# Kernel optimization log

Hardware: AMD Instinct MI355X
Metric: run time of the kernel (lower is better)

Reference implementation:

```python
import jax, jax.numpy as jnp
import numpy as np

T, N = 8192, 1024
W_MEAN, W_VAR = 0.2, 0.4


def setup_inputs() -> dict:
    key = jax.random.key(0)
    k_x, k_w = jax.random.split(key, 2)
    x_in = jax.random.normal(k_x, (T, N), dtype=jnp.float32) * 5.0
    # w ~ U(w_mean - w_var, w_mean + w_var), matching the torch init
    w = W_MEAN - W_VAR + 2.0 * W_VAR * jax.random.uniform(k_w, (N, N), dtype=jnp.float32)
    ones = jnp.ones((N,), jnp.float32)
    return {
        "x_in": x_in,
        "w": w,
        "E_L": -54.0 * ones,
        "tau_m": 1.4 * ones,
        "G": 0.7 * ones,
        "R_I": 132.0 * ones,
        "f_v": 0.3 * ones,
        "f_I": 0.6 * ones,
        "delta_theta_s": 11.0 * ones,
        "b_s": 0.3 * ones,
        "a_v": 0.3 * ones,
        "b_v": 0.3 * ones,
        "theta_inf": -24.5 * ones,
        "delta_V": 10.0 * ones,
        "I_A": 1.6 * ones,
    }


def reference(x_in, w, E_L, tau_m, G, R_I, f_v, f_I, delta_theta_s, b_s,
              a_v, b_v, theta_inf, delta_V, I_A):
    n = w.shape[0]
    # self_recurrence_mask = ones(N,N) - eye(N)
    w_masked = w * (1.0 - jnp.eye(n, dtype=w.dtype))

    def step(carry, x):
        v, theta_s, theta_v, I_add = carry
        I = I_add @ w_masked + 0.85 * x  # [N] recurrent drive + scaled input
        v_next = v + (I * R_I - G * (v - E_L)) / tau_m
        thr = theta_s + theta_v
        spiked_soft = jax.nn.sigmoid(v_next - thr)  # surrogate spike (self.spiked)
        spiked = (v_next >= thr).astype(v.dtype)    # hard spike
        not_spiked = 1.0 - spiked
        v_reset = E_L + f_v * (v - E_L) - delta_V
        v_new = spiked * v_reset + not_spiked * v_next
        theta_s_new = (1.0 - b_s) * theta_s + spiked * delta_theta_s
        d_theta_v = a_v * (v_new - E_L) - b_v * (theta_v - theta_inf)
        theta_v_new = theta_v + not_spiked * d_theta_v
        I_add_new = (1.0 - f_I) * I_add + spiked_soft * I_A
        return (v_new, theta_s_new, theta_v_new, I_add_new), (v_new, spiked_soft)

    init = (E_L,                               # v = E_L * ones(N)
            30.0 * jnp.ones_like(E_L),         # theta_s
            jnp.ones_like(E_L),                # theta_v
            jnp.zeros_like(E_L))               # I_additive
    _, (vs, spikes) = jax.lax.scan(step, init, x_in)
    return vs, spikes  # each [T, N]
```

## Files before the change

### kernel.cpp

```cpp
#include <hip/hip_runtime.h>


#define T_STEPS 8192
#define N_NEUR  1024
#define NBLK    32
#define TPB     256
#define PSTRIDE (NBLK * N_NEUR)

typedef unsigned long long ull;

__global__ void glif_init(ull* __restrict__ buf) {
    int i = blockIdx.x * blockDim.x + threadIdx.x;
    if (i < PSTRIDE) {
        buf[i] = 0ULL;
    } else if (i < 2 * PSTRIDE) {
        buf[i] = 0xFFFFFFFF00000000ULL;
    }
}

__launch_bounds__(TPB, 1)
__global__ void glif_main(const float* __restrict__ x_in,
                          const float* __restrict__ w_p,
                          const float* __restrict__ E_L_p,
                          const float* __restrict__ tau_m_p,
                          const float* __restrict__ G_p,
                          const float* __restrict__ R_I_p,
                          const float* __restrict__ f_v_p,
                          const float* __restrict__ f_I_p,
                          const float* __restrict__ dths_p,
                          const float* __restrict__ b_s_p,
                          const float* __restrict__ a_v_p,
                          const float* __restrict__ b_v_p,
                          const float* __restrict__ th_inf_p,
                          const float* __restrict__ dV_p,
                          const float* __restrict__ I_A_p,
                          float* __restrict__ out,
                          ull* __restrict__ buf) {
    const int tid  = threadIdx.x;
    const int wv   = tid >> 6;
    const int lane = tid & 63;
    const int colL = lane & 31;
    const int col  = blockIdx.x * 32 + colL;
    const int ibase = wv * 256 + (lane >> 5) * 128;

    __shared__ float ix[N_NEUR];
    __shared__ float red[4][32];

    float wreg[128];
#pragma unroll
    for (int j = 0; j < 128; ++j) {
        int r = ibase + j;
        float wval = w_p[(size_t)r * N_NEUR + col];
        wreg[j] = (r == col) ? 0.0f : wval;
    }

    const bool own = (lane < 32);
    float E_L = 0.f, inv_tau = 0.f, Gc = 0.f, R_I = 0.f, f_v = 0.f, om_fI = 0.f;
    float dths = 0.f, om_bs = 0.f, a_v = 0.f, b_v = 0.f, th_inf = 0.f, dV = 0.f, I_A = 0.f;
    float v = 0.f, th_s = 0.f, th_v = 0.f, I_own = 0.f, xnext = 0.f;
    if (own) {
        E_L     = E_L_p[col];
        inv_tau = 1.0f / tau_m_p[col];
        Gc      = G_p[col];
        R_I     = R_I_p[col];
        f_v     = f_v_p[col];
        om_fI   = 1.0f - f_I_p[col];
        dths    = dths_p[col];
        om_bs   = 1.0f - b_s_p[col];
        a_v     = a_v_p[col];
        b_v     = b_v_p[col];
        th_inf  = th_inf_p[col];
        dV      = dV_p[col];
        I_A     = I_A_p[col];
        v = E_L; th_s = 30.0f; th_v = 1.0f; I_own = 0.0f;
        xnext = x_in[col];
    }

    float* __restrict__ vs_out = out;
    float* __restrict__ sp_out = out + (size_t)T_STEPS * N_NEUR;

    for (int t = 0; t < T_STEPS; ++t) {
        const ull* src = buf + (size_t)(t & 1) * PSTRIDE
                             + (size_t)blockIdx.x * N_NEUR + tid * 4;
        ull u0, u1, u2, u3;
        const unsigned ut = (unsigned)t;
        for (;;) {
            asm volatile(
                "global_load_dwordx2 %0, %4, off sc0 sc1\n\t"
                "global_load_dwordx2 %1, %4, off offset:8 sc0 sc1\n\t"
                "global_load_dwordx2 %2, %4, off offset:16 sc0 sc1\n\t"
                "global_load_dwordx2 %3, %4, off offset:24 sc0 sc1\n\t"
                "s_waitcnt vmcnt(0)"
                : "=&v"(u0), "=&v"(u1), "=&v"(u2), "=&v"(u3)
                : "v"(src)
                : "memory");
            bool ok = ((unsigned)(u0 >> 32) == ut) & ((unsigned)(u1 >> 32) == ut) &
                      ((unsigned)(u2 >> 32) == ut) & ((unsigned)(u3 >> 32) == ut);
            if (ok) break;
        }
        ((float4*)ix)[tid] = make_float4(__uint_as_float((unsigned)u0),
                                         __uint_as_float((unsigned)u1),
                                         __uint_as_float((unsigned)u2),
                                         __uint_as_float((unsigned)u3));

        asm volatile("s_waitcnt lgkmcnt(0)" ::: "memory");
        __builtin_amdgcn_s_barrier();
        __builtin_amdgcn_sched_barrier(0);

        float xt = xnext;
        if (own) {
            int tn = (t + 1 < T_STEPS) ? (t + 1) : t;
            xnext = x_in[(size_t)tn * N_NEUR + col];
        }

        float s0 = 0.f, s1 = 0.f, s2 = 0.f, s3 = 0.f;
        const float4* q4 = (const float4*)(ix + ibase);
#pragma unroll
        for (int m = 0; m < 32; ++m) {
            float4 q = q4[m];
            s0 = fmaf(wreg[4 * m + 0], q.x, s0);
            s1 = fmaf(wreg[4 * m + 1], q.y, s1);
            s2 = fmaf(wreg[4 * m + 2], q.z, s2);
            s3 = fmaf(wreg[4 * m + 3], q.w, s3);
        }
        float acc = (s0 + s1) + (s2 + s3);
        acc += __shfl_xor(acc, 32, 64);
        if (lane < 32) red[wv][colL] = acc;

        asm volatile("s_waitcnt lgkmcnt(0)" ::: "memory");
        __builtin_amdgcn_s_barrier();
        __builtin_amdgcn_sched_barrier(0);

        if (own) {
            float I = (red[0][colL] + red[1][colL]) + (red[2][colL] + red[3][colL])
                      + 0.85f * xt;
            float v_next = v + (I * R_I - Gc * (v - E_L)) * inv_tau;
            float thr = th_s + th_v;
            float z = v_next - thr;
            float soft = 1.0f / (1.0f + __expf(-z));
            I_own = om_fI * I_own + soft * I_A;

            ull pk = ((ull)(unsigned)(t + 1) << 32) | (ull)__float_as_uint(I_own);
            ull* dst = buf + (size_t)((t + 1) & 1) * PSTRIDE
                           + (size_t)(wv * 8) * N_NEUR + col;
#pragma unroll
            for (int k = 0; k < 8; ++k) {
                __hip_atomic_store(dst + (size_t)k * N_NEUR, pk,
                                   __ATOMIC_RELAXED, __HIP_MEMORY_SCOPE_AGENT);
            }

            bool  sp = (v_next >= thr);
            float v_reset = E_L + f_v * (v - E_L) - dV;
            float v_new = sp ? v_reset : v_next;
            th_s = om_bs * th_s + (sp ? dths : 0.0f);
            float d_thv = a_v * (v_new - E_L) - b_v * (th_v - th_inf);
            th_v = th_v + (sp ? 0.0f : d_thv);
            v = v_new;

            if (wv == 0) {
                __builtin_nontemporal_store(v_new, &vs_out[(size_t)t * N_NEUR + col]);
                __builtin_nontemporal_store(soft, &sp_out[(size_t)t * N_NEUR + col]);
            }
        }
    }
}

extern "C" void kernel_launch(void* const* d_in, const int* in_sizes, int n_in,
                              void* d_out, int out_size, void* d_ws, size_t ws_size,
                              hipStream_t stream) {
    const float* x_in   = (const float*)d_in[0];
    const float* w      = (const float*)d_in[1];
    const float* E_L    = (const float*)d_in[2];
    const float* tau_m  = (const float*)d_in[3];
    const float* G      = (const float*)d_in[4];
    const float* R_I    = (const float*)d_in[5];
    const float* f_v    = (const float*)d_in[6];
    const float* f_I    = (const float*)d_in[7];
    const float* dths   = (const float*)d_in[8];
    const float* b_s    = (const float*)d_in[9];
    const float* a_v    = (const float*)d_in[10];
    const float* b_v    = (const float*)d_in[11];
    const float* th_inf = (const float*)d_in[12];
    const float* dV     = (const float*)d_in[13];
    const float* I_A    = (const float*)d_in[14];

    float* out = (float*)d_out;
    ull* buf = (ull*)d_ws;

    glif_init<<<(2 * PSTRIDE + TPB - 1) / TPB, TPB, 0, stream>>>(buf);
    glif_main<<<NBLK, TPB, 0, stream>>>(x_in, w, E_L, tau_m, G, R_I, f_v, f_I,
                                        dths, b_s, a_v, b_v, th_inf, dV, I_A,
                                        out, buf);
}
```

Before: 15.83 ms.

## Add dedicated wave for neuron state update and publishing, separate from matvec waves

Grows the block from four waves to five. The first four waves only poll the exchange buffer, run the recurrent dot products and write partial sums. The new fifth wave owns the per-neuron state update, sigmoid, output stores and the next-step x_in prefetch. It publishes I_add with 16 atomic stores per lane instead of 8 stores spread over four waves. The aim is to take the serial tail work off the matvec waves so they can go straight back to polling, at the cost of more store issue on a single wave in the critical path.

Measured after the change: 18.21 ms. 15.0% more time.

```diff
diff --git a/kernel.cpp b/kernel.cpp
--- a/kernel.cpp
+++ b/kernel.cpp
@@ -4,7 +4,7 @@
 #define T_STEPS 8192
 #define N_NEUR  1024
 #define NBLK    32
-#define TPB     256
+#define TPB     320
 #define PSTRIDE (NBLK * N_NEUR)
 
 typedef unsigned long long ull;
@@ -39,99 +39,100 @@
     const int tid  = threadIdx.x;
     const int wv   = tid >> 6;
     const int lane = tid & 63;
-    const int colL = lane & 31;
-    const int col  = blockIdx.x * 32 + colL;
-    const int ibase = wv * 256 + (lane >> 5) * 128;
 
     __shared__ float ix[N_NEUR];
     __shared__ float red[4][32];
 
-    float wreg[128];
-#pragma unroll
-    for (int j = 0; j < 128; ++j) {
-        int r = ibase + j;
-        float wval = w_p[(size_t)r * N_NEUR + col];
-        wreg[j] = (r == col) ? 0.0f : wval;
-    }
-
-    const bool own = (lane < 32);
-    float E_L = 0.f, inv_tau = 0.f, Gc = 0.f, R_I = 0.f, f_v = 0.f, om_fI = 0.f;
-    float dths = 0.f, om_bs = 0.f, a_v = 0.f, b_v = 0.f, th_inf = 0.f, dV = 0.f, I_A = 0.f;
-    float v = 0.f, th_s = 0.f, th_v = 0.f, I_own = 0.f, xnext = 0.f;
-    if (own) {
-        E_L     = E_L_p[col];
-        inv_tau = 1.0f / tau_m_p[col];
-        Gc      = G_p[col];
-        R_I     = R_I_p[col];
-        f_v     = f_v_p[col];
-        om_fI   = 1.0f - f_I_p[col];
-        dths    = dths_p[col];
-        om_bs   = 1.0f - b_s_p[col];
-        a_v     = a_v_p[col];
-        b_v     = b_v_p[col];
-        th_inf  = th_inf_p[col];
-        dV      = dV_p[col];
-        I_A     = I_A_p[col];
-        v = E_L; th_s = 30.0f; th_v = 1.0f; I_own = 0.0f;
-        xnext = x_in[col];
-    }
-
     float* __restrict__ vs_out = out;
     float* __restrict__ sp_out = out + (size_t)T_STEPS * N_NEUR;
 
-    for (int t = 0; t < T_STEPS; ++t) {
-        const ull* src = buf + (size_t)(t & 1) * PSTRIDE
-                             + (size_t)blockIdx.x * N_NEUR + tid * 4;
-        ull u0, u1, u2, u3;
-        const unsigned ut = (unsigned)t;
-        for (;;) {
-            asm volatile(
-                "global_load_dwordx2 %0, %4, off sc0 sc1\n\t"
-                "global_load_dwordx2 %1, %4, off offset:8 sc0 sc1\n\t"
-                "global_load_dwordx2 %2, %4, off offset:16 sc0 sc1\n\t"
-                "global_load_dwordx2 %3, %4, off offset:24 sc0 sc1\n\t"
-                "s_waitcnt vmcnt(0)"
-                : "=&v"(u0), "=&v"(u1), "=&v"(u2), "=&v"(u3)
-                : "v"(src)
-                : "memory");
-            bool ok = ((unsigned)(u0 >> 32) == ut) & ((unsigned)(u1 >> 32) == ut) &
-                      ((unsigned)(u2 >> 32) == ut) & ((unsigned)(u3 >> 32) == ut);
-            if (ok) break;
-        }
-        ((float4*)ix)[tid] = make_float4(__uint_as_float((unsigned)u0),
-                                         __uint_as_float((unsigned)u1),
-                                         __uint_as_float((unsigned)u2),
-                                         __uint_as_float((unsigned)u3));
+    if (wv < 4) {
+        const int colL  = lane & 31;
+        const int col   = blockIdx.x * 32 + colL;
+        const int ibase = wv * 256 + (lane >> 5) * 128;
 
-        asm volatile("s_waitcnt lgkmcnt(0)" ::: "memory");
-        __builtin_amdgcn_s_barrier();
-        __builtin_amdgcn_sched_barrier(0);
-
-        float xt = xnext;
-        if (own) {
-            int tn = (t + 1 < T_STEPS) ? (t + 1) : t;
-            xnext = x_in[(size_t)tn * N_NEUR + col];
+        float wreg[128];
+#pragma unroll
+        for (int j = 0; j < 128; ++j) {
+            int r = ibase + j;
+            float wval = w_p[(size_t)r * N_NEUR + col];
+            wreg[j] = (r == col) ? 0.0f : wval;
         }
 
-        float s0 = 0.f, s1 = 0.f, s2 = 0.f, s3 = 0.f;
-        const float4* q4 = (const float4*)(ix + ibase);
+        for (int t = 0; t < T_STEPS; ++t) {
+            const ull* src = buf + (size_t)(t & 1) * PSTRIDE
+                                 + (size_t)blockIdx.x * N_NEUR + tid * 4;
+            ull u0, u1, u2, u3;
+            const unsigned ut = (unsigned)t;
+            for (;;) {
+                asm volatile(
+                    "global_load_dwordx2 %0, %4, off sc0 sc1\n\t"
+                    "global_load_dwordx2 %1, %4, off offset:8 sc0 sc1\n\t"
+                    "global_load_dwordx2 %2, %4, off offset:16 sc0 sc1\n\t"
+                    "global_load_dwordx2 %3, %4, off offset:24 sc0 sc1\n\t"
+                    "s_waitcnt vmcnt(0)"
+                    : "=&v"(u0), "=&v"(u1), "=&v"(u2), "=&v"(u3)
+                    : "v"(src)
+                    : "memory");
+                bool ok = ((unsigned)(u0 >> 32) == ut) & ((unsigned)(u1 >> 32) == ut) &
+                          ((unsigned)(u2 >> 32) == ut) & ((unsigned)(u3 >> 32) == ut);
+                if (ok) break;
+            }
+            ((float4*)ix)[tid] = make_float4(__uint_as_float((unsigned)u0),
+                                             __uint_as_float((unsigned)u1),
+                                             __uint_as_float((unsigned)u2),
+                                             __uint_as_float((unsigned)u3));
+
+            asm volatile("s_waitcnt lgkmcnt(0)" ::: "memory");
+            __builtin_amdgcn_s_barrier();
+            __builtin_amdgcn_sched_barrier(0);
+
+            float s0 = 0.f, s1 = 0.f, s2 = 0.f, s3 = 0.f;
+            const float4* q4 = (const float4*)(ix + ibase);
 #pragma unroll
-        for (int m = 0; m < 32; ++m) {
-            float4 q = q4[m];
-            s0 = fmaf(wreg[4 * m + 0], q.x, s0);
-            s1 = fmaf(wreg[4 * m + 1], q.y, s1);
-            s2 = fmaf(wreg[4 * m + 2], q.z, s2);
-            s3 = fmaf(wreg[4 * m + 3], q.w, s3);
+            for (int m = 0; m < 32; ++m) {
+                float4 q = q4[m];
+                s0 = fmaf(wreg[4 * m + 0], q.x, s0);
+                s1 = fmaf(wreg[4 * m + 1], q.y, s1);
+                s2 = fmaf(wreg[4 * m + 2], q.z, s2);
+                s3 = fmaf(wreg[4 * m + 3], q.w, s3);
+            }
+            float acc = (s0 + s1) + (s2 + s3);
+            acc += __shfl_xor(acc, 32, 64);
+            if (lane < 32) red[wv][colL] = acc;
+
+            asm volatile("s_waitcnt lgkmcnt(0)" ::: "memory");
+            __builtin_amdgcn_s_barrier();
+            __builtin_amdgcn_sched_barrier(0);
         }
-        float acc = (s0 + s1) + (s2 + s3);
-        acc += __shfl_xor(acc, 32, 64);
-        if (lane < 32) red[wv][colL] = acc;
+    } else {
+        const int h    = lane >> 5;
+        const int colL = lane & 31;
+        const int col  = blockIdx.x * 32 + colL;
 
-        asm volatile("s_waitcnt lgkmcnt(0)" ::: "memory");
-        __builtin_amdgcn_s_barrier();
-        __builtin_amdgcn_sched_barrier(0);
+        const float E_L     = E_L_p[col];
+        const float inv_tau = 1.0f / tau_m_p[col];
+        const float Gc      = G_p[col];
+        const float R_I     = R_I_p[col];
+        const float f_v     = f_v_p[col];
+        const float om_fI   = 1.0f - f_I_p[col];
+        const float dths    = dths_p[col];
+        const float om_bs   = 1.0f - b_s_p[col];
+        const float a_v     = a_v_p[col];
+        const float b_v     = b_v_p[col];
+        const float th_inf  = th_inf_p[col];
+        const float dV      = dV_p[col];
+        const float I_A     = I_A_p[col];
 
-        if (own) {
+        float v = E_L, th_s = 30.0f, th_v = 1.0f, I_own = 0.0f;
+        float xnext = x_in[col];
+
+        for (int t = 0; t < T_STEPS; ++t) {
+            __builtin_amdgcn_s_barrier();
+            __builtin_amdgcn_s_barrier();
+            __builtin_amdgcn_sched_barrier(0);
+
+            float xt = xnext;
             float I = (red[0][colL] + red[1][colL]) + (red[2][colL] + red[3][colL])
                       + 0.85f * xt;
             float v_next = v + (I * R_I - Gc * (v - E_L)) * inv_tau;
@@ -142,9 +143,9 @@
 
             ull pk = ((ull)(unsigned)(t + 1) << 32) | (ull)__float_as_uint(I_own);
             ull* dst = buf + (size_t)((t + 1) & 1) * PSTRIDE
-                           + (size_t)(wv * 8) * N_NEUR + col;
+                           + (size_t)(h * 16) * N_NEUR + col;
 #pragma unroll
-            for (int k = 0; k < 8; ++k) {
+            for (int k = 0; k < 16; ++k) {
                 __hip_atomic_store(dst + (size_t)k * N_NEUR, pk,
                                    __ATOMIC_RELAXED, __HIP_MEMORY_SCOPE_AGENT);
             }
@@ -157,10 +158,12 @@
             th_v = th_v + (sp ? 0.0f : d_thv);
             v = v_new;
 
-            if (wv == 0) {
+            if (h == 0) {
                 __builtin_nontemporal_store(v_new, &vs_out[(size_t)t * N_NEUR + col]);
                 __builtin_nontemporal_store(soft, &sp_out[(size_t)t * N_NEUR + col]);
             }
+            int tn = (t + 1 < T_STEPS) ? (t + 1) : t;
+            xnext = x_in[(size_t)tn * N_NEUR + col];
         }
     }
 }
@@ -187,7 +190,7 @@
     float* out = (float*)d_out;
     ull* buf = (ull*)d_ws;
 
-    glif_init<<<(2 * PSTRIDE + TPB - 1) / TPB, TPB, 0, stream>>>(buf);
+    glif_init<<<(2 * PSTRIDE + 255) / 256, 256, 0, stream>>>(buf);
     glif_main<<<NBLK, TPB, 0, stream>>>(x_in, w, E_L, tau_m, G, R_I, f_v, f_I,
                                         dths, b_s, a_v, b_v, th_inf, dV, I_A,
                                         out, buf);
```
